# Performance work log

Measured on AMD Instinct MI355X. Metric: run time of the kernel, lower is better.

The kernel has to match this reference:

```python
import jax, jax.numpy as jnp
import numpy as np

N = 131072      # nodes
E = 524288      # edges (avg degree 4)
F_IN = 16       # node features (QM9-like)
DIM = 64        # GRU hidden / lin0 out
DNN = 16        # NNConv channels
BK = 4          # bond kinds (edge_attr dim)
NG = 8192       # graphs in batch
NL1 = 4         # number of GRUs
NL2 = 2         # inner repeats per GRU


def setup_inputs() -> dict:
    key = jax.random.key(0)
    ks = jax.random.split(key, 16)
    s = 0.1
    inp = {}
    inp["x"] = jax.random.normal(ks[0], (N, F_IN), jnp.float32)
    inp["edge_attr"] = jax.random.uniform(ks[1], (E, BK), dtype=jnp.float32)
    # lin0: F_IN -> DIM
    inp["lin0_w"] = jax.random.normal(ks[2], (F_IN, DIM), jnp.float32) * s
    inp["lin0_b"] = jnp.zeros((DIM,), jnp.float32)
    # nn1: BK -> DNN*DNN (per-edge weight generator)
    inp["nn1_w"] = jax.random.normal(ks[3], (BK, DNN * DNN), jnp.float32) * s
    inp["nn1_b"] = jax.random.normal(ks[4], (DNN * DNN,), jnp.float32) * s
    # NNConv root weight + bias
    inp["root_w"] = jax.random.normal(ks[5], (DNN, DNN), jnp.float32) * s
    inp["conv_b"] = jnp.zeros((DNN,), jnp.float32)
    # 4 GRUs, each input=DNN, hidden=DIM (torch layout: [3*DIM, in])
    inp["gru_w_ih"] = jax.random.normal(ks[6], (NL1, 3 * DIM, DNN), jnp.float32) * s
    inp["gru_w_hh"] = jax.random.normal(ks[7], (NL1, 3 * DIM, DIM), jnp.float32) * s
    inp["gru_b_ih"] = jax.random.normal(ks[8], (NL1, 3 * DIM), jnp.float32) * s
    inp["gru_b_hh"] = jax.random.normal(ks[9], (NL1, 3 * DIM), jnp.float32) * s
    # lin1_64_16 and lin_64_1 (no bias)
    inp["lin1_w"] = jax.random.normal(ks[10], (DIM, DNN), jnp.float32) * s
    inp["lin1_b"] = jnp.zeros((DNN,), jnp.float32)
    inp["lin2_w"] = jax.random.normal(ks[11], (DIM, 1), jnp.float32) * s
    inp["edge_index"] = jax.random.randint(ks[12], (2, E), 0, N, jnp.int32)
    inp["batch"] = jnp.sort(jax.random.randint(ks[13], (N,), 0, NG, jnp.int32))
    return inp


def reference(x, edge_attr, lin0_w, lin0_b, nn1_w, nn1_b, root_w, conv_b,
              gru_w_ih, gru_w_hh, gru_b_ih, gru_b_hh, lin1_w, lin1_b, lin2_w,
              edge_index, batch):
    n = x.shape[0]
    src, dst = edge_index[0], edge_index[1]
    # precompute mean-aggregation denominators (in-degree, clamped at 1)
    cnt = jax.ops.segment_sum(jnp.ones((edge_index.shape[1],), x.dtype), dst,
                              num_segments=n)
    inv_cnt = (1.0 / jnp.maximum(cnt, 1.0))[:, None]          # [N,1]
    # per-edge 16x16 weights from edge features (shared across all iterations)
    W_e = (edge_attr @ nn1_w + nn1_b).reshape(-1, DNN, DNN)   # [E,16,16]

    def nnconv(xi):  # xi: [N,16]
        msg = jnp.einsum('ei,eio->eo', xi[src], W_e)          # gather + per-edge matmul
        aggr = jax.ops.segment_sum(msg, dst, num_segments=n) * inv_cnt  # scatter-mean
        return xi @ root_w + aggr + conv_b

    def gru_step(j, xin, h):  # xin: [N,16], h: [N,64]
        gi = xin @ gru_w_ih[j].T + gru_b_ih[j]                # [N,192]
        gh = h @ gru_w_hh[j].T + gru_b_hh[j]                  # [N,192]
        i_r, i_z, i_n = jnp.split(gi, 3, axis=-1)
        h_r, h_z, h_n = jnp.split(gh, 3, axis=-1)
        r = jax.nn.sigmoid(i_r + h_r)
        z = jax.nn.sigmoid(i_z + h_z)
        ncand = jnp.tanh(i_n + r * h_n)
        return (1.0 - z) * ncand + z * h

    out = jax.nn.relu(x @ lin0_w + lin0_b)                    # [N,64]
    h = out
    for j in range(NL1):
        for _ in range(NL2):
            out1 = out @ lin1_w + lin1_b                      # [N,16]
            out2 = nnconv(out1)                               # [N,16]
            h = gru_step(j, out2, h)
            out = h
    y = out @ lin2_w                                          # [N,1]
    pooled = jax.ops.segment_sum(y, batch, num_segments=NG)   # global_add_pool
    return pooled.reshape(-1)
```

## Files before the change

### kernel.cpp

```cpp
#include <hip/hip_runtime.h>
#include <hip/hip_bf16.h>

#define N_NODES 131072
#define N_EDGES 524288
#define F_IN 16
#define DIM 64
#define DNN 16
#define BK 4
#define NG 8192
#define N_ITERS 8

typedef __bf16 bf16x8 __attribute__((ext_vector_type(8)));
typedef __bf16 bf16x4 __attribute__((ext_vector_type(4)));
typedef float f32x4 __attribute__((ext_vector_type(4)));

#define FMA4(A_, S_, W_) { (A_).x = fmaf((S_), (W_).x, (A_).x); (A_).y = fmaf((S_), (W_).y, (A_).y); \
                           (A_).z = fmaf((S_), (W_).z, (A_).z); (A_).w = fmaf((S_), (W_).w, (A_).w); }

__device__ __forceinline__ unsigned bf16_rne(float f) {
    unsigned u = __float_as_uint(f);
    return (u + 0x7fffu + ((u >> 16) & 1u)) >> 16;
}

__global__ __launch_bounds__(256) void k_degree(const int* __restrict__ ei, int* __restrict__ cnt) {
    int e = blockIdx.x * 256 + threadIdx.x;
    atomicAdd(&cnt[ei[N_EDGES + e]], 1);
}

__global__ __launch_bounds__(256) void k_invcnt(const int* __restrict__ cnt, float* __restrict__ inv) {
    int i = blockIdx.x * 256 + threadIdx.x;
    inv[i] = 1.0f / (float)max(cnt[i], 1);
}

__global__ __launch_bounds__(256) void k_scanA(const int* __restrict__ cnt, int* __restrict__ excl,
                                               int* __restrict__ bsum) {
    __shared__ int a[256], b[256];
    int t = threadIdx.x, gid = blockIdx.x * 256 + t;
    int c = cnt[gid];
    a[t] = c; __syncthreads();
    int *s = a, *d = b;
#pragma unroll
    for (int off = 1; off < 256; off <<= 1) {
        d[t] = s[t] + (t >= off ? s[t - off] : 0);
        __syncthreads();
        int* tmp = s; s = d; d = tmp;
    }
    excl[gid] = s[t] - c;
    if (t == 255) bsum[blockIdx.x] = s[255];
}

__global__ __launch_bounds__(256) void k_scanB(const int* __restrict__ bsum, int* __restrict__ boff) {
    __shared__ int a[512], b[512];
    int t = threadIdx.x;
    a[t] = bsum[t]; a[t + 256] = bsum[t + 256];
    __syncthreads();
    int *s = a, *d = b;
#pragma unroll
    for (int off = 1; off < 512; off <<= 1) {
        d[t] = s[t] + (t >= off ? s[t - off] : 0);
        int i2 = t + 256;
        d[i2] = s[i2] + (i2 >= off ? s[i2 - off] : 0);
        __syncthreads();
        int* tmp = s; s = d; d = tmp;
    }
    boff[t] = t ? s[t - 1] : 0;
    boff[t + 256] = s[t + 255];
}

__global__ __launch_bounds__(256) void k_scanC(const int* __restrict__ excl, const int* __restrict__ boff,
                                               int* __restrict__ row_ptr, int* __restrict__ cursor) {
    int gid = blockIdx.x * 256 + threadIdx.x;
    int v = excl[gid] + boff[gid >> 8];
    row_ptr[gid] = v;
    cursor[gid] = v;
    if (gid == 0) row_ptr[N_NODES] = N_EDGES;
}

__global__ __launch_bounds__(256) void k_scatter(const int* __restrict__ ei, const float* __restrict__ ea,
                                                 int* __restrict__ cursor, int4* __restrict__ csr_pk) {
    int e = blockIdx.x * 256 + threadIdx.x;
    int dst = ei[N_EDGES + e];
    int pos = atomicAdd(&cursor[dst], 1);
    float4 a = ((const float4*)ea)[e];
    unsigned a01 = bf16_rne(a.x) | (bf16_rne(a.y) << 16);
    unsigned a23 = bf16_rne(a.z) | (bf16_rne(a.w) << 16);
    csr_pk[pos] = make_int4(ei[e], (int)a01, (int)a23, 0);
}

#define WB_SZ (4 * 40 * 512)
__global__ __launch_bounds__(256) void k_prep(const float* __restrict__ wih, const float* __restrict__ whh,
                                              const float* __restrict__ rw, const float* __restrict__ w1,
                                              const float* __restrict__ bih, const float* __restrict__ bhh,
                                              const float* __restrict__ nn1w, const float* __restrict__ nn1b,
                                              __bf16* __restrict__ Wb, __bf16* __restrict__ B2b,
                                              __bf16* __restrict__ w1b) {
    int idx = blockIdx.x * 256 + threadIdx.x;
    if (idx < WB_SZ) {
        int j = idx / 20480, r = idx % 20480;
        int t = r >> 9, e = r & 511;
        int jj = e & 7, c16 = (e >> 3) & 15, kq = e >> 7;
        int ct, kk; bool nih = false;
        if (t < 36) { ct = t / 3; kk = t % 3; } else { ct = 8 + (t - 36); kk = 0; nih = true; }
        int k = kk * 32 + kq * 8 + jj;
        int c = ct * 16 + c16;
        bool ngate = ct >= 8;
        float v = 0.f;
        if (nih) {
            if (k < 16) v = wih[((size_t)j * 192 + c) * 16 + k];
        } else {
            if (k < 16) v = ngate ? 0.f : wih[((size_t)j * 192 + c) * 16 + k];
            else if (k < 80) v = whh[((size_t)j * 192 + c) * 64 + (k - 16)];
            else if (k == 80) v = ngate ? bhh[j * 192 + c] : (bih[j * 192 + c] + bhh[j * 192 + c]);
        }
        Wb[idx] = (__bf16)v;
    } else if (idx < WB_SZ + 1536) {
        int e = idx - WB_SZ;
        int t = e >> 9, ee = e & 511;
        int jj = ee & 7, c16 = (ee >> 3) & 15, kq = ee >> 7;
        int krow = t * 32 + kq * 8 + jj;
        float v;
        if (krow < 16) v = rw[krow * 16 + c16];
        else {
            int i = (krow - 16) >> 4, kk = (krow - 16) & 15;
            v = (i == 0) ? nn1b[kk * 16 + c16] : nn1w[(i - 1) * 256 + kk * 16 + c16];
        }
        B2b[e] = (__bf16)v;
    } else if (idx < WB_SZ + 1536 + 1024) {
        int e = idx - (WB_SZ + 1536);
        int t2 = e >> 9, ee = e & 511;
        int jj = ee & 7, c16 = (ee >> 3) & 15, kq = ee >> 7;
        int k = t2 * 32 + kq * 8 + jj;
        w1b[e] = (__bf16)w1[k * 16 + c16];
    }
}

__global__ __launch_bounds__(256) void k_init(const float* __restrict__ x, const float* __restrict__ w,
                                              const float* __restrict__ b, __bf16* __restrict__ h) {
    __shared__ float s_w[F_IN * DIM];
    int tid = threadIdx.x;
    for (int i = tid; i < F_IN * DIM; i += 256) s_w[i] = w[i];
    int node = blockIdx.x * 16 + (tid >> 4);
    int c4 = tid & 15;
    const float4* xp = (const float4*)(x + (size_t)node * F_IN);
    float4 x0 = xp[0], x1 = xp[1], x2 = xp[2], x3 = xp[3];
    float xa[16] = {x0.x, x0.y, x0.z, x0.w, x1.x, x1.y, x1.z, x1.w,
                    x2.x, x2.y, x2.z, x2.w, x3.x, x3.y, x3.z, x3.w};
    __syncthreads();
    float4 acc = ((const float4*)b)[c4];
    const float4* w4 = (const float4*)s_w;
#pragma unroll
    for (int k = 0; k < 16; ++k) {
        float4 wv = w4[k * 16 + c4];
        FMA4(acc, xa[k], wv);
    }
    bf16x4 hv;
    hv[0] = (__bf16)fmaxf(acc.x, 0.f); hv[1] = (__bf16)fmaxf(acc.y, 0.f);
    hv[2] = (__bf16)fmaxf(acc.z, 0.f); hv[3] = (__bf16)fmaxf(acc.w, 0.f);
    *(bf16x4*)&h[(size_t)node * DIM + c4 * 4] = hv;
}

__global__ __launch_bounds__(256) void k_lin1(const __bf16* __restrict__ h, const float* __restrict__ w,
                                              const float* __restrict__ b, __bf16* __restrict__ out1) {
    __shared__ float s_h[64 * 68];
    int tid = threadIdx.x;
    int nb = blockIdx.x * 64;
    for (int i = tid; i < 64 * 16; i += 256) {
        int n = i >> 4, q4 = i & 15;
        bf16x4 v = *(const bf16x4*)&h[(size_t)(nb + n) * 64 + q4 * 4];
        float* d = &s_h[n * 68 + q4 * 4];
        d[0] = (float)v[0]; d[1] = (float)v[1]; d[2] = (float)v[2]; d[3] = (float)v[3];
    }
    int ct = tid & 15;
    float wcol[64];
#pragma unroll
    for (int q = 0; q < 64; ++q) wcol[q] = w[q * 16 + ct];
    float bias = b[ct];
    __syncthreads();
    int ng = tid >> 4;
#pragma unroll
    for (int rep = 0; rep < 4; ++rep) {
        int nl = ng + 16 * rep;
        float acc = bias;
#pragma unroll
        for (int q4 = 0; q4 < 16; ++q4) {
            float4 hv = *(const float4*)&s_h[nl * 68 + q4 * 4];
            acc = fmaf(hv.x, wcol[4 * q4 + 0], acc);
            acc = fmaf(hv.y, wcol[4 * q4 + 1], acc);
            acc = fmaf(hv.z, wcol[4 * q4 + 2], acc);
            acc = fmaf(hv.w, wcol[4 * q4 + 3], acc);
        }
        out1[(size_t)(nb + nl) * 16 + ct] = (__bf16)acc;
    }
}

__attribute__((amdgpu_waves_per_eu(2, 4)))
__global__ __launch_bounds__(512) void k_node(
    const __bf16* __restrict__ out1_in, __bf16* __restrict__ out1_out,
    const int4* __restrict__ csr_pk,
    const int* __restrict__ row_ptr, const float* __restrict__ inv_cnt,
    __bf16* __restrict__ h, const __bf16* __restrict__ Wb, const __bf16* __restrict__ B2b,
    const __bf16* __restrict__ w1b, const float* __restrict__ conv_b,
    const float* __restrict__ bih, const float* __restrict__ lin1_b,
    const int* __restrict__ batch, const float* __restrict__ lin2_w,
    float* __restrict__ out, int do_final)
{
    __shared__ __align__(16) __bf16 s_X[128 * 104];
    __shared__ __align__(16) __bf16 s_W[40 * 512];
    __shared__ __align__(16) __bf16 s_B2[3 * 512];
    __shared__ __align__(16) __bf16 s_w1[1024];
    int tid = threadIdx.x;
    int nb = blockIdx.x * 128;
    int lane = tid & 63, w = tid >> 6;
    int c16 = lane & 15, lq = lane >> 4;
    int nwb = nb + w * 16;
    int xrow = w * 16;

    {
        const float4* src = (const float4*)Wb;
        float4* dst = (float4*)s_W;
#pragma unroll
        for (int i = 0; i < 5; ++i) dst[tid + 512 * i] = src[tid + 512 * i];
        if (tid < 192) ((float4*)s_B2)[tid] = ((const float4*)B2b)[tid];
        else if (tid < 320) ((float4*)s_w1)[tid - 192] = ((const float4*)w1b)[tid - 192];
    }
    {
        int n = lane >> 2, k4 = lane & 3;
        bf16x4 v = *(const bf16x4*)&out1_in[(size_t)(nwb + n) * 16 + k4 * 4];
        *(bf16x4*)&s_X[(xrow + n) * 104 + k4 * 4] = v;
    }
    __syncthreads();

    {
        int gi = lane >> 4, k = lane & 15;
        int e0[4], dr[4];
        int4 pk[4];
        float S0[4] = {0.f,0.f,0.f,0.f}, S1[4] = {0.f,0.f,0.f,0.f}, S2[4] = {0.f,0.f,0.f,0.f},
              S3[4] = {0.f,0.f,0.f,0.f}, S4[4] = {0.f,0.f,0.f,0.f};
        int rounds = 0;
#pragma unroll
        for (int r = 0; r < 4; ++r) {
            int n = nwb + gi * 4 + r;
            e0[r] = row_ptr[n];
            dr[r] = row_ptr[n + 1] - e0[r];
            rounds = max(rounds, dr[r]);
            pk[r] = csr_pk[min(e0[r], N_EDGES - 1)];
        }
        for (int t = 0; t < rounds; ++t) {
            int4 pkn[4]; float xv[4];
#pragma unroll
            for (int r = 0; r < 4; ++r)
                pkn[r] = csr_pk[min(e0[r] + t + 1, N_EDGES - 1)];
#pragma unroll
            for (int r = 0; r < 4; ++r)
                xv[r] = (float)out1_in[(size_t)(pk[r].x & 0xFFFFF) * 16 + k];
#pragma unroll
            for (int r = 0; r < 4; ++r) {
                float xm = (t < dr[r]) ? xv[r] : 0.0f;
                float a0 = __uint_as_float(((unsigned)pk[r].y) << 16);
                float a1 = __uint_as_float(((unsigned)pk[r].y) & 0xffff0000u);
                float a2 = __uint_as_float(((unsigned)pk[r].z) << 16);
                float a3 = __uint_as_float(((unsigned)pk[r].z) & 0xffff0000u);
                S0[r] += xm;
                S1[r] = fmaf(a0, xm, S1[r]);
                S2[r] = fmaf(a1, xm, S2[r]);
                S3[r] = fmaf(a2, xm, S3[r]);
                S4[r] = fmaf(a3, xm, S4[r]);
                pk[r] = pkn[r];
            }
        }
#pragma unroll
        for (int r = 0; r < 4; ++r) {
            int nl = xrow + gi * 4 + r;
            float inv = inv_cnt[nwb + gi * 4 + r];
            __bf16* p = &s_X[nl * 104];
            p[16 + k] = (__bf16)(S0[r] * inv);
            p[32 + k] = (__bf16)(S1[r] * inv);
            p[48 + k] = (__bf16)(S2[r] * inv);
            p[64 + k] = (__bf16)(S3[r] * inv);
            p[80 + k] = (__bf16)(S4[r] * inv);
        }
    }

    float cb = conv_b[c16];
    f32x4 co2 = (f32x4){cb, cb, cb, cb};
#pragma unroll
    for (int kk = 0; kk < 3; ++kk) {
        bf16x8 a = *(const bf16x8*)&s_X[(xrow + c16) * 104 + kk * 32 + lq * 8];
        bf16x8 b = *(const bf16x8*)&s_B2[kk * 512 + lane * 8];
        co2 = __builtin_amdgcn_mfma_f32_16x16x32_bf16(a, b, co2, 0, 0, 0);
    }

#pragma unroll
    for (int jr = 0; jr < 4; ++jr)
        s_X[(xrow + 4 * lq + jr) * 104 + c16] = (__bf16)co2[jr];
    {
        const bf16x8* hsrc = (const bf16x8*)(h + (size_t)nwb * 64);
#pragma unroll
        for (int ii = 0; ii < 2; ++ii) {
            int idx = lane + 64 * ii;
            int n = idx >> 3, d8 = idx & 7;
            bf16x8 v = hsrc[idx];
            *(bf16x8*)&s_X[(xrow + n) * 104 + 16 + d8 * 8] = v;
        }
    }
    {
        int n = lane >> 2, c0 = 80 + (lane & 3) * 4;
#pragma unroll
        for (int q = 0; q < 4; ++q)
            s_X[(xrow + n) * 104 + c0 + q] = (c0 + q == 80) ? (__bf16)1.0f : (__bf16)0.0f;
    }

    f32x4 acc[12], ani4[4];
#pragma unroll
    for (int i = 0; i < 12; ++i) acc[i] = (f32x4){0.f, 0.f, 0.f, 0.f};
#pragma unroll
    for (int i = 0; i < 4; ++i) ani4[i] = (f32x4){0.f, 0.f, 0.f, 0.f};
    bf16x8 af[3];
#pragma unroll
    for (int kk = 0; kk < 3; ++kk)
        af[kk] = *(const bf16x8*)&s_X[(xrow + c16) * 104 + kk * 32 + lq * 8];
#pragma unroll
    for (int ct = 0; ct < 12; ++ct) {
#pragma unroll
        for (int kk = 0; kk < 3; ++kk) {
            bf16x8 bf = *(const bf16x8*)&s_W[(ct * 3 + kk) * 512 + lane * 8];
            acc[ct] = __builtin_amdgcn_mfma_f32_16x16x32_bf16(af[kk], bf, acc[ct], 0, 0, 0);
        }
    }
#pragma unroll
    for (int ct8 = 0; ct8 < 4; ++ct8) {
        bf16x8 bf = *(const bf16x8*)&s_W[(36 + ct8) * 512 + lane * 8];
        ani4[ct8] = __builtin_amdgcn_mfma_f32_16x16x32_bf16(af[0], bf, ani4[ct8], 0, 0, 0);
    }

    float hn[4][4];
#pragma unroll
    for (int ct = 0; ct < 4; ++ct) {
        float bni = bih[128 + ct * 16 + c16];
#pragma unroll
        for (int jr = 0; jr < 4; ++jr) {
            float hold = (float)s_X[(xrow + 4 * lq + jr) * 104 + 16 + ct * 16 + c16];
            float rr = 1.f / (1.f + __expf(-acc[ct][jr]));
            float zz = 1.f / (1.f + __expf(-acc[4 + ct][jr]));
            float xx = fmaf(rr, acc[8 + ct][jr], ani4[ct][jr] + bni);
            float ax = fabsf(xx);
            float ee = __expf(-2.f * ax);
            float ncv = __builtin_copysignf((1.f - ee) / (1.f + ee), xx);
            hn[ct][jr] = fmaf(zz, hold - ncv, ncv);
        }
    }
#pragma unroll
    for (int ct = 0; ct < 4; ++ct)
#pragma unroll
        for (int jr = 0; jr < 4; ++jr)
            s_X[(xrow + 4 * lq + jr) * 104 + 16 + ct * 16 + c16] = (__bf16)hn[ct][jr];
    {
        bf16x8* hdst = (bf16x8*)(h + (size_t)nwb * 64);
#pragma unroll
        for (int ii = 0; ii < 2; ++ii) {
            int idx = lane + 64 * ii;
            int n = idx >> 3, d8 = idx & 7;
            bf16x8 v = *(const bf16x8*)&s_X[(xrow + n) * 104 + 16 + d8 * 8];
            hdst[idx] = v;
        }
    }

    if (!do_final) {
        f32x4 o1acc = (f32x4){0.f, 0.f, 0.f, 0.f};
#pragma unroll
        for (int kk = 0; kk < 2; ++kk) {
            bf16x8 a = *(const bf16x8*)&s_X[(xrow + c16) * 104 + 16 + kk * 32 + lq * 8];
            bf16x8 b = *(const bf16x8*)&s_w1[kk * 512 + lane * 8];
            o1acc = __builtin_amdgcn_mfma_f32_16x16x32_bf16(a, b, o1acc, 0, 0, 0);
        }
        float lb = lin1_b[c16];
#pragma unroll
        for (int jr = 0; jr < 4; ++jr) {
            int node = nwb + 4 * lq + jr;
            out1_out[(size_t)node * 16 + c16] = (__bf16)(o1acc[jr] + lb);
        }
    } else {
        float w2v[4];
#pragma unroll
        for (int ct = 0; ct < 4; ++ct) w2v[ct] = lin2_w[ct * 16 + c16];
#pragma unroll
        for (int jr = 0; jr < 4; ++jr) {
            float part = hn[0][jr] * w2v[0];
            part = fmaf(hn[1][jr], w2v[1], part);
            part = fmaf(hn[2][jr], w2v[2], part);
            part = fmaf(hn[3][jr], w2v[3], part);
#pragma unroll
            for (int off = 8; off > 0; off >>= 1) part += __shfl_xor(part, off, 64);
            if (c16 == 0) {
                int node = nwb + 4 * lq + jr;
                atomicAdd(&out[batch[node]], part);
            }
        }
    }
}

extern "C" void kernel_launch(void* const* d_in, const int* in_sizes, int n_in,
                              void* d_out, int out_size, void* d_ws, size_t ws_size,
                              hipStream_t stream) {
    const float* x        = (const float*)d_in[0];
    const float* edge_attr= (const float*)d_in[1];
    const float* lin0_w   = (const float*)d_in[2];
    const float* lin0_b   = (const float*)d_in[3];
    const float* nn1_w    = (const float*)d_in[4];
    const float* nn1_b    = (const float*)d_in[5];
    const float* root_w   = (const float*)d_in[6];
    const float* conv_b   = (const float*)d_in[7];
    const float* gru_w_ih = (const float*)d_in[8];
    const float* gru_w_hh = (const float*)d_in[9];
    const float* gru_b_ih = (const float*)d_in[10];
    const float* gru_b_hh = (const float*)d_in[11];
    const float* lin1_w   = (const float*)d_in[12];
    const float* lin1_b   = (const float*)d_in[13];
    const float* lin2_w   = (const float*)d_in[14];
    const int*   ei       = (const int*)d_in[15];
    const int*   batch    = (const int*)d_in[16];
    float* out = (float*)d_out;

    char* p = (char*)d_ws;
    __bf16* h       = (__bf16*)p;           p += (size_t)N_NODES * DIM * 2;
    __bf16* out1A   = (__bf16*)p;           p += (size_t)N_NODES * DNN * 2;
    __bf16* out1B   = (__bf16*)p;           p += (size_t)N_NODES * DNN * 2;
    int4*   csr_pk  = (int4*)p;             p += (size_t)N_EDGES * 16;
    __bf16* Wb      = (__bf16*)p;           p += (size_t)WB_SZ * 2;
    __bf16* B2b     = (__bf16*)p;           p += 1536 * 2;
    __bf16* w1b     = (__bf16*)p;           p += 1024 * 2;
    int*    cnt     = (int*)p;              p += (size_t)N_NODES * 4;
    float*  inv_cnt = (float*)p;            p += (size_t)N_NODES * 4;
    int*    row_ptr = (int*)p;              p += (size_t)(N_NODES + 16) * 4;
    int*    cursor  = (int*)p;              p += (size_t)N_NODES * 4;
    int*    excl    = (int*)p;              p += (size_t)N_NODES * 4;
    int*    bsum    = (int*)p;              p += 512 * 4;
    int*    boff    = (int*)p;              p += 512 * 4;

    hipMemsetAsync(d_out, 0, (size_t)NG * 4, stream);
    hipMemsetAsync(cnt, 0, (size_t)N_NODES * 4, stream);
    k_prep<<<330, 256, 0, stream>>>(gru_w_ih, gru_w_hh, root_w, lin1_w, gru_b_ih, gru_b_hh,
                                    nn1_w, nn1_b, Wb, B2b, w1b);
    k_degree<<<N_EDGES / 256, 256, 0, stream>>>(ei, cnt);
    k_scanA<<<N_NODES / 256, 256, 0, stream>>>(cnt, excl, bsum);
    k_scanB<<<1, 256, 0, stream>>>(bsum, boff);
    k_scanC<<<N_NODES / 256, 256, 0, stream>>>(excl, boff, row_ptr, cursor);
    k_scatter<<<N_EDGES / 256, 256, 0, stream>>>(ei, edge_attr, cursor, csr_pk);
    k_invcnt<<<N_NODES / 256, 256, 0, stream>>>(cnt, inv_cnt);
    k_init<<<N_NODES / 16, 256, 0, stream>>>(x, lin0_w, lin0_b, h);
    k_lin1<<<N_NODES / 64, 256, 0, stream>>>(h, lin1_w, lin1_b, out1A);

    for (int it = 0; it < N_ITERS; ++it) {
        int j = it >> 1;
        const __bf16* o_in = (it & 1) ? out1B : out1A;
        __bf16*       o_out= (it & 1) ? out1A : out1B;
        k_node<<<N_NODES / 128, 512, 0, stream>>>(o_in, o_out, csr_pk, row_ptr, inv_cnt,
                                                  h, Wb + (size_t)j * 40 * 512, B2b, w1b,
                                                  conv_b, gru_b_ih + (size_t)j * 192, lin1_b,
                                                  batch, lin2_w, out, it == N_ITERS - 1 ? 1 : 0);
    }
}
```

Before: 403.9 us.

## Renumber nodes by descending in-degree to balance edge work per wavefront

Adds a counting-sort pass (histogram, bin offsets, atomic permute) that assigns each node a slot ordered by in-degree, then builds the CSR, hidden state, inverse counts and batch ids in slot order. The node kernel then processes nodes with similar degrees together, which reduces divergence and tail imbalance in the per-node edge loops. In exchange, node locality from the original ordering is lost: consecutive pooled atomics now hit scattered graph ids and source gathers become more random. Several small setup kernels are also added.

```diff
diff --git a/kernel.cpp b/kernel.cpp
--- a/kernel.cpp
+++ b/kernel.cpp
@@ -27,9 +27,32 @@
     atomicAdd(&cnt[ei[N_EDGES + e]], 1);
 }
 
-__global__ __launch_bounds__(256) void k_invcnt(const int* __restrict__ cnt, float* __restrict__ inv) {
-    int i = blockIdx.x * 256 + threadIdx.x;
-    inv[i] = 1.0f / (float)max(cnt[i], 1);
+__global__ __launch_bounds__(256) void k_hist(const int* __restrict__ cnt, int* __restrict__ hist) {
+    int n = blockIdx.x * 256 + threadIdx.x;
+    int key = 31 - min(cnt[n], 31);
+    atomicAdd(&hist[key], 1);
+}
+
+__global__ __launch_bounds__(64) void k_binoff(const int* __restrict__ hist, int* __restrict__ binoff) {
+    if (threadIdx.x == 0) {
+        int acc = 0;
+#pragma unroll
+        for (int i = 0; i < 32; ++i) { binoff[i] = acc; acc += hist[i]; }
+    }
+}
+
+__global__ __launch_bounds__(256) void k_permute(const int* __restrict__ cnt, const int* __restrict__ binoff,
+                                                 int* __restrict__ bincur, const int* __restrict__ batch,
+                                                 int* __restrict__ slot_of, int* __restrict__ cnts,
+                                                 float* __restrict__ invs, int* __restrict__ batchs) {
+    int n = blockIdx.x * 256 + threadIdx.x;
+    int deg = cnt[n];
+    int key = 31 - min(deg, 31);
+    int slot = binoff[key] + atomicAdd(&bincur[key], 1);
+    slot_of[n] = slot;
+    cnts[slot] = deg;
+    invs[slot] = 1.0f / (float)max(deg, 1);
+    batchs[slot] = batch[n];
 }
 
 __global__ __launch_bounds__(256) void k_scanA(const int* __restrict__ cnt, int* __restrict__ excl,
@@ -77,14 +100,15 @@
 }
 
 __global__ __launch_bounds__(256) void k_scatter(const int* __restrict__ ei, const float* __restrict__ ea,
+                                                 const int* __restrict__ slot_of,
                                                  int* __restrict__ cursor, int4* __restrict__ csr_pk) {
     int e = blockIdx.x * 256 + threadIdx.x;
-    int dst = ei[N_EDGES + e];
-    int pos = atomicAdd(&cursor[dst], 1);
+    int ds = slot_of[ei[N_EDGES + e]];
+    int pos = atomicAdd(&cursor[ds], 1);
     float4 a = ((const float4*)ea)[e];
     unsigned a01 = bf16_rne(a.x) | (bf16_rne(a.y) << 16);
     unsigned a23 = bf16_rne(a.z) | (bf16_rne(a.w) << 16);
-    csr_pk[pos] = make_int4(ei[e], (int)a01, (int)a23, 0);
+    csr_pk[pos] = make_int4(slot_of[ei[e]], (int)a01, (int)a23, 0);
 }
 
 #define WB_SZ (4 * 40 * 512)
@@ -135,7 +159,8 @@
 }
 
 __global__ __launch_bounds__(256) void k_init(const float* __restrict__ x, const float* __restrict__ w,
-                                              const float* __restrict__ b, __bf16* __restrict__ h) {
+                                              const float* __restrict__ b, const int* __restrict__ slot_of,
+                                              __bf16* __restrict__ h) {
     __shared__ float s_w[F_IN * DIM];
     int tid = threadIdx.x;
     for (int i = tid; i < F_IN * DIM; i += 256) s_w[i] = w[i];
@@ -156,7 +181,8 @@
     bf16x4 hv;
     hv[0] = (__bf16)fmaxf(acc.x, 0.f); hv[1] = (__bf16)fmaxf(acc.y, 0.f);
     hv[2] = (__bf16)fmaxf(acc.z, 0.f); hv[3] = (__bf16)fmaxf(acc.w, 0.f);
-    *(bf16x4*)&h[(size_t)node * DIM + c4 * 4] = hv;
+    int s = slot_of[node];
+    *(bf16x4*)&h[(size_t)s * DIM + c4 * 4] = hv;
 }
 
 __global__ __launch_bounds__(256) void k_lin1(const __bf16* __restrict__ h, const float* __restrict__ w,
@@ -197,11 +223,11 @@
 __global__ __launch_bounds__(512) void k_node(
     const __bf16* __restrict__ out1_in, __bf16* __restrict__ out1_out,
     const int4* __restrict__ csr_pk,
-    const int* __restrict__ row_ptr, const float* __restrict__ inv_cnt,
+    const int* __restrict__ row_ptr, const float* __restrict__ invs,
     __bf16* __restrict__ h, const __bf16* __restrict__ Wb, const __bf16* __restrict__ B2b,
     const __bf16* __restrict__ w1b, const float* __restrict__ conv_b,
     const float* __restrict__ bih, const float* __restrict__ lin1_b,
-    const int* __restrict__ batch, const float* __restrict__ lin2_w,
+    const int* __restrict__ batchs, const float* __restrict__ lin2_w,
     float* __restrict__ out, int do_final)
 {
     __shared__ __align__(16) __bf16 s_X[128 * 104];
@@ -271,7 +297,7 @@
 #pragma unroll
         for (int r = 0; r < 4; ++r) {
             int nl = xrow + gi * 4 + r;
-            float inv = inv_cnt[nwb + gi * 4 + r];
+            float inv = invs[nwb + gi * 4 + r];
             __bf16* p = &s_X[nl * 104];
             p[16 + k] = (__bf16)(S0[r] * inv);
             p[32 + k] = (__bf16)(S1[r] * inv);
@@ -393,7 +419,7 @@
             for (int off = 8; off > 0; off >>= 1) part += __shfl_xor(part, off, 64);
             if (c16 == 0) {
                 int node = nwb + 4 * lq + jr;
-                atomicAdd(&out[batch[node]], part);
+                atomicAdd(&out[batchs[node]], part);
             }
         }
     }
@@ -430,33 +456,44 @@
     __bf16* B2b     = (__bf16*)p;           p += 1536 * 2;
     __bf16* w1b     = (__bf16*)p;           p += 1024 * 2;
     int*    cnt     = (int*)p;              p += (size_t)N_NODES * 4;
-    float*  inv_cnt = (float*)p;            p += (size_t)N_NODES * 4;
+    float*  invs    = (float*)p;            p += (size_t)N_NODES * 4;
     int*    row_ptr = (int*)p;              p += (size_t)(N_NODES + 16) * 4;
     int*    cursor  = (int*)p;              p += (size_t)N_NODES * 4;
     int*    excl    = (int*)p;              p += (size_t)N_NODES * 4;
     int*    bsum    = (int*)p;              p += 512 * 4;
     int*    boff    = (int*)p;              p += 512 * 4;
+    int*    slot_of = (int*)p;              p += (size_t)N_NODES * 4;
+    int*    cnts    = (int*)p;              p += (size_t)N_NODES * 4;
+    int*    batchs  = (int*)p;              p += (size_t)N_NODES * 4;
+    int*    hist    = (int*)p;              p += 32 * 4;
+    int*    binoff  = (int*)p;              p += 32 * 4;
+    int*    bincur  = (int*)p;              p += 32 * 4;
 
     hipMemsetAsync(d_out, 0, (size_t)NG * 4, stream);
     hipMemsetAsync(cnt, 0, (size_t)N_NODES * 4, stream);
+    hipMemsetAsync(hist, 0, 32 * 4, stream);
+    hipMemsetAsync(bincur, 0, 32 * 4, stream);
     k_prep<<<330, 256, 0, stream>>>(gru_w_ih, gru_w_hh, root_w, lin1_w, gru_b_ih, gru_b_hh,
                                     nn1_w, nn1_b, Wb, B2b, w1b);
     k_degree<<<N_EDGES / 256, 256, 0, stream>>>(ei, cnt);
-    k_scanA<<<N_NODES / 256, 256, 0, stream>>>(cnt, excl, bsum);
+    k_hist<<<N_NODES / 256, 256, 0, stream>>>(cnt, hist);
+    k_binoff<<<1, 64, 0, stream>>>(hist, binoff);
+    k_permute<<<N_NODES / 256, 256, 0, stream>>>(cnt, binoff, bincur, batch,
+                                                 slot_of, cnts, invs, batchs);
+    k_scanA<<<N_NODES / 256, 256, 0, stream>>>(cnts, excl, bsum);
     k_scanB<<<1, 256, 0, stream>>>(bsum, boff);
     k_scanC<<<N_NODES / 256, 256, 0, stream>>>(excl, boff, row_ptr, cursor);
-    k_scatter<<<N_EDGES / 256, 256, 0, stream>>>(ei, edge_attr, cursor, csr_pk);
-    k_invcnt<<<N_NODES / 256, 256, 0, stream>>>(cnt, inv_cnt);
-    k_init<<<N_NODES / 16, 256, 0, stream>>>(x, lin0_w, lin0_b, h);
+    k_scatter<<<N_EDGES / 256, 256, 0, stream>>>(ei, edge_attr, slot_of, cursor, csr_pk);
+    k_init<<<N_NODES / 16, 256, 0, stream>>>(x, lin0_w, lin0_b, slot_of, h);
     k_lin1<<<N_NODES / 64, 256, 0, stream>>>(h, lin1_w, lin1_b, out1A);
 
     for (int it = 0; it < N_ITERS; ++it) {
         int j = it >> 1;
         const __bf16* o_in = (it & 1) ? out1B : out1A;
         __bf16*       o_out= (it & 1) ? out1A : out1B;
-        k_node<<<N_NODES / 128, 512, 0, stream>>>(o_in, o_out, csr_pk, row_ptr, inv_cnt,
+        k_node<<<N_NODES / 128, 512, 0, stream>>>(o_in, o_out, csr_pk, row_ptr, invs,
                                                   h, Wb + (size_t)j * 40 * 512, B2b, w1b,
                                                   conv_b, gru_b_ih + (size_t)j * 192, lin1_b,
-                                                  batch, lin2_w, out, it == N_ITERS - 1 ? 1 : 0);
-    }
-}
+                                                  batchs, lin2_w, out, it == N_ITERS - 1 ? 1 : 0);
+    }
+}
```

Measured after the change: 1.421 ms. +251.9%, slower.
